# Kernel optimization log

Hardware: AMD Instinct MI355X
Metric: run time of the kernel (lower is better)

The kernel has to match this reference:

```python
import jax, jax.numpy as jnp
import numpy as np

C = 1024        # number of classes
N = 8           # proxies per class
ALLNUM = C * N  # 8192 total proxies
DIM = 512
R = 0.05
TOPK = int(np.ceil(R * ALLNUM))  # 410
LAM = 0.3
B = 2048


def setup_inputs() -> dict:
    key = jax.random.key(0)
    k1, k2, k3 = jax.random.split(key, 3)
    inp = jax.random.normal(k1, (B, DIM), dtype=jnp.float32)
    target = jax.random.randint(k2, (B,), 0, C, dtype=jnp.int64)
    # kaiming-uniform-initialized proxies approximated by scaled normal init
    proxies = jax.random.normal(k3, (DIM, ALLNUM), dtype=jnp.float32)
    instance_label = jnp.repeat(jnp.arange(C, dtype=jnp.int64), N)  # [ALLNUM]
    return {"input": inp, "target": target, "Proxies": proxies,
            "instance_label": instance_label}


def reference(input, target, Proxies, instance_label):
    # L2-normalize each proxy column (F.normalize along dim=0, eps=1e-12)
    norm = jnp.maximum(jnp.linalg.norm(Proxies, axis=0, keepdims=True), 1e-12)
    centers = Proxies / norm                             # [DIM, ALLNUM]
    similarity = input @ centers                          # [B, ALLNUM]

    positive_mask = (target[:, None] == instance_label[None, :]).astype(similarity.dtype)
    _, indices = jax.lax.top_k(similarity + 1000.0 * positive_mask, TOPK)  # [B, TOPK]

    rows = jnp.arange(similarity.shape[0])[:, None]
    mask = jnp.zeros_like(similarity).at[rows, indices].set(1.0)
    prob_a = mask * similarity                            # sparse-masked similarities

    y_instance_onehot = jax.nn.one_hot(instance_label, C, dtype=similarity.dtype)  # [ALLNUM, C]
    logits = prob_a @ y_instance_onehot                   # [B, C]

    y_target_onehot = jax.nn.one_hot(target, C, dtype=similarity.dtype)  # [B, C]
    logits_mask = 1.0 - (logits == 0.0).astype(similarity.dtype)

    # scale_mask_softmax with scale=1 along dim=1
    e = jnp.exp(logits) * logits_mask
    predict = e / (1e-8 + jnp.sum(e, axis=1, keepdims=True))
    lossClassify = jnp.mean(jnp.sum(-y_target_onehot * jnp.log(predict + 1e-20), axis=1))

    # proxy regularizer: cross-entropy of proxy-vs-class logits
    simCenter = centers.T @ centers                       # [ALLNUM, ALLNUM]
    centers_logits = simCenter @ y_instance_onehot        # [ALLNUM, C]
    logp = jax.nn.log_softmax(centers_logits, axis=1)
    reg = -jnp.mean(jnp.take_along_axis(logp, instance_label[:, None], axis=1))

    return (lossClassify + LAM * reg, lossClassify)
```

## Files before the change

kernel.cpp:

```cpp
#include <hip/hip_runtime.h>
#include <hip/hip_bf16.h>
#include <math.h>

#define C_CLS   1024
#define NPROXY  8
#define ALLNUM  8192
#define DIM     512
#define TOPK    410
#define LAM     0.3f
#define BATCH   2048

#define BAND_CAP_BLK 40
#define ROW_CAP      512
#define GCAP         64

typedef __bf16 bf16x8 __attribute__((ext_vector_type(8)));
typedef float floatx4 __attribute__((ext_vector_type(4)));
typedef unsigned short ushort_t;

#define WS_RNORM 0
#define WS_SIG   8192
#define WS_LP    10240
#define WS_RP    12288
#define WS_CNT   14336
#define WS_NDEF  16384
#define WS_FLAG  18432
#define WS_CLS   20480
#define WS_BVAL  (WS_CLS + 2048*1024)
#define WS_BCOL  (WS_BVAL + 2048*512)
#define WS_ABF   (WS_BCOL + 2048*256)
#define WS_PBF   (WS_ABF + 524288)
#define WS_STBF  (WS_PBF + 2097152)
#define WS_LOG   (WS_STBF + 262144)

__device__ inline float block_reduce(float v, int is_max, float* red, int t) {
    #pragma unroll
    for (int o = 32; o > 0; o >>= 1) {
        float w = __shfl_down(v, o);
        v = is_max ? fmaxf(v, w) : (v + w);
    }
    __syncthreads();
    if ((t & 63) == 0) red[t >> 6] = v;
    __syncthreads();
    return is_max ? fmaxf(fmaxf(red[0], red[1]), fmaxf(red[2], red[3]))
                  : (red[0] + red[1] + red[2] + red[3]);
}

__device__ inline ushort_t f2bf(float f) {
    unsigned u = __float_as_uint(f);
    return (ushort_t)((u + 0x7FFFu + ((u >> 16) & 1u)) >> 16);
}

__device__ inline float bf2f(ushort_t u) {
    return __uint_as_float(((unsigned)u) << 16);
}

__device__ inline void ld_g2l_16(const void* g, void* l) {
    __builtin_amdgcn_global_load_lds(
        (const __attribute__((address_space(1))) unsigned int*)g,
        (__attribute__((address_space(3))) unsigned int*)l,
        16, 0, 0);
}

__device__ inline unsigned f2ord(float f) {
    unsigned u = __float_as_uint(f);
    return (u & 0x80000000u) ? ~u : (u | 0x80000000u);
}

__global__ __launch_bounds__(256) void k_prep1(const float* __restrict__ P,
                                               const float* __restrict__ input,
                                               float* __restrict__ rnorm,
                                               float* __restrict__ rowsig,
                                               ushort_t* __restrict__ Abf,
                                               ushort_t* __restrict__ Pbf,
                                               ushort_t* __restrict__ Stbf,
                                               unsigned* __restrict__ zaux) {
    __shared__ float tile[32][33];
    __shared__ float s_rn[32];
    float* cred = &tile[0][0];
    int bx = blockIdx.x, t = threadIdx.x;
    if (bx < 256) {
        int tc = t & 31, g = t >> 5;
        int c = bx * 32 + tc;
        const float* pc = P + (size_t)(g * 64) * ALLNUM + c;
        float s = 0.f;
        #pragma unroll 8
        for (int d = 0; d < 64; ++d) {
            float v = pc[(size_t)d * ALLNUM];
            s += v * v;
        }
        cred[g * 32 + tc] = s;
        __syncthreads();
        if (g == 0) {
            float tot = 0.f;
            #pragma unroll
            for (int k = 0; k < 8; ++k) tot += cred[k * 32 + tc];
            float r = 1.0f / fmaxf(sqrtf(tot), 1e-12f);
            rnorm[c] = r;
            s_rn[tc] = r;
        }
        __syncthreads();
        #pragma unroll
        for (int p = 0; p < 8; ++p) {
            int idx = t + 256 * p;
            int d = idx >> 2, cc = idx & 3;
            const float* pp = P + (size_t)d * ALLNUM + bx * 32 + cc * 8;
            const float* rr = &s_rn[cc * 8];
            float4 a = *(const float4*)pp;
            float4 b = *(const float4*)(pp + 4);
            float v = a.x * rr[0] + a.y * rr[1] + a.z * rr[2] + a.w * rr[3] +
                      b.x * rr[4] + b.y * rr[5] + b.z * rr[6] + b.w * rr[7];
            Stbf[(size_t)(bx * 4 + cc) * DIM + d] = f2bf(v);
        }
    } else if (bx < 256 + 1024) {
        int a = bx - 256;
        int idx = a * 256 + t;
        float4 v = ((const float4*)input)[idx];
        ushort4 o;
        o.x = f2bf(v.x); o.y = f2bf(v.y); o.z = f2bf(v.z); o.w = f2bf(v.w);
        ((ushort4*)Abf)[idx] = o;
        float sq = v.x * v.x + v.y * v.y + v.z * v.z + v.w * v.w;
        #pragma unroll
        for (int off = 32; off > 0; off >>= 1) sq += __shfl_down(sq, off);
        int lane = t & 63, w = t >> 6;
        if (lane == 0) cred[w] = sq;
        __syncthreads();
        if (t == 0) {
            rowsig[2 * a]     = sqrtf(cred[0] + cred[1]);
            rowsig[2 * a + 1] = sqrtf(cred[2] + cred[3]);
        }
    } else if (bx < 256 + 1024 + 4096) {
        int id = bx - 1280;
        int c0 = (id & 255) * 32, r0 = (id >> 8) * 32;
        int tc = t & 31, tr = t >> 5;
        #pragma unroll
        for (int p = 0; p < 4; ++p)
            tile[tr + p * 8][tc] = P[(size_t)(r0 + tr + p * 8) * ALLNUM + c0 + tc];
        __syncthreads();
        #pragma unroll
        for (int p = 0; p < 4; ++p) {
            int oc = tr + p * 8;
            Pbf[(size_t)(c0 + oc) * DIM + r0 + tc] = f2bf(tile[tc][oc]);
        }
    } else {
        for (int i = t; i < 3 * 2048; i += 256) zaux[i] = 0u;
    }
}

__global__ __launch_bounds__(512, 2) void k_gemms(const ushort_t* __restrict__ Abf,
                                                  const ushort_t* __restrict__ Pbf,
                                                  const ushort_t* __restrict__ Stbf,
                                                  const float* __restrict__ rnorm,
                                                  const float* __restrict__ rowsig,
                                                  const int* __restrict__ target,
                                                  float* __restrict__ g_cls,
                                                  float* __restrict__ g_bval,
                                                  ushort_t* __restrict__ g_bcol,
                                                  unsigned* __restrict__ g_cnt,
                                                  unsigned* __restrict__ g_ndef,
                                                  unsigned* __restrict__ g_flag,
                                                  ushort_t* __restrict__ logits) {
    __shared__ __align__(16) ushort_t smem[65536];
    int bx = blockIdx.x, t = threadIdx.x;
    int w = t >> 6, lane = t & 63;
    int ml = lane & 15, q4 = lane >> 4;

    if (bx < 256) {
        int bi = (bx >> 5) * 256, bj = (bx & 31) * 256;
        int wm = w >> 2, wn = w & 3;
        ushort_t* sA0 = smem;
        ushort_t* sB0 = smem + 16384;
        ushort_t* sA1 = smem + 32768;
        ushort_t* sB1 = smem + 49152;

        floatx4 acc[8][4];
        #pragma unroll
        for (int mf = 0; mf < 8; ++mf)
            #pragma unroll
            for (int nf = 0; nf < 4; ++nf)
                acc[mf][nf] = (floatx4){0.f, 0.f, 0.f, 0.f};

        #define STAGE0(sa, sb, k0) do {                                        \
            _Pragma("unroll")                                                  \
            for (int it = 0; it < 4; ++it) {                                   \
                int c = w * 256 + it * 64 + lane;                              \
                int m = c >> 3, s = c & 7, qq = s ^ (m & 7);                   \
                ld_g2l_16(Abf + ((size_t)(bi + m) << 9) + (k0) + qq * 8,       \
                          &(sa)[c * 8]);                                       \
            }                                                                  \
            _Pragma("unroll")                                                  \
            for (int it = 0; it < 4; ++it) {                                   \
                int c = w * 256 + it * 64 + lane;                              \
                int m = c >> 3, s = c & 7, qq = s ^ (m & 7);                   \
                ld_g2l_16(Pbf + ((size_t)(bj + m) << 9) + (k0) + qq * 8,       \
                          &(sb)[c * 8]);                                       \
            }                                                                  \
        } while (0)

        STAGE0(sA0, sB0, 0);
        __syncthreads();
        #pragma unroll
        for (int tt = 0; tt < 8; ++tt) {
            ushort_t* cA = (tt & 1) ? sA1 : sA0;
            ushort_t* cB = (tt & 1) ? sB1 : sB0;
            if (tt < 7) {
                if (tt & 1) STAGE0(sA0, sB0, (tt + 1) * 64);
                else        STAGE0(sA1, sB1, (tt + 1) * 64);
            }
            #pragma unroll
            for (int kk = 0; kk < 2; ++kk) {
                bf16x8 bfr[4];
                #pragma unroll
                for (int nf = 0; nf < 4; ++nf) {
                    int n = wn * 64 + nf * 16 + ml;
                    int s = (kk * 4 + q4) ^ (n & 7);
                    bfr[nf] = *(const bf16x8*)&cB[n * 64 + s * 8];
                }
                #pragma unroll
                for (int mf = 0; mf < 8; ++mf) {
                    int m = wm * 128 + mf * 16 + ml;
                    int s = (kk * 4 + q4) ^ (m & 7);
                    bf16x8 af = *(const bf16x8*)&cA[m * 64 + s * 8];
                    #pragma unroll
                    for (int nf = 0; nf < 4; ++nf)
                        acc[mf][nf] = __builtin_amdgcn_mfma_f32_16x16x32_bf16(
                            af, bfr[nf], acc[mf][nf], 0, 0, 0);
                }
            }
            __syncthreads();
        }

        unsigned char* sb8 = (unsigned char*)smem;
        float*    e_cls = (float*)sb8;
        float*    e_bv  = (float*)(sb8 + 32768);
        ushort_t* e_bc  = (ushort_t*)(sb8 + 73728);
        unsigned* e_cnt = (unsigned*)(sb8 + 94208);
        unsigned* e_nd  = (unsigned*)(sb8 + 95232);

        #pragma unroll
        for (int i = t; i < 8192; i += 512) e_cls[i] = 0.f;
        if (t < 256) { e_cnt[t] = 0u; e_nd[t] = 0u; }
        __syncthreads();

        #pragma unroll
        for (int mf = 0; mf < 8; ++mf) {
            int rl0 = wm * 128 + mf * 16 + q4 * 4;
            int rowb = bi + rl0;
            float4 rs4 = *(const float4*)&rowsig[rowb];
            int4   tg4 = *(const int4*)&target[rowb];
            #pragma unroll
            for (int nf = 0; nf < 4; ++nf) {
                int cl = wn * 64 + nf * 16 + ml;
                int col = bj + cl;
                float sc = rnorm[col];
                int cls = col >> 3;
                int clsl = cl >> 3;
                #pragma unroll
                for (int i = 0; i < 4; ++i) {
                    int rl = rl0 + i;
                    float v = acc[mf][nf][i] * sc;
                    float sg = ((const float*)&rs4)[i] * (1.0f / 22.616f);
                    float hiT = 1.80f * sg, loT = 1.47f * sg;
                    int tg = ((const int*)&tg4)[i];
                    if (cls == tg) {
                        atomicAdd(&e_cls[rl * 32 + clsl], v);
                    } else if (v >= hiT) {
                        atomicAdd(&e_cls[rl * 32 + clsl], v);
                        atomicAdd(&e_nd[rl], 1u);
                    } else if (v >= loT) {
                        unsigned u = atomicAdd(&e_cnt[rl], 1u);
                        if (u < BAND_CAP_BLK) {
                            e_bv[rl * BAND_CAP_BLK + u] = v;
                            e_bc[rl * BAND_CAP_BLK + u] = (ushort_t)col;
                        }
                    }
                }
            }
        }
        __syncthreads();

        int bjc = bj >> 3;
        #pragma unroll
        for (int i = t; i < 8192; i += 512) {
            int rl = i >> 5, c = i & 31;
            g_cls[(size_t)(bi + rl) * C_CLS + bjc + c] = e_cls[i];
        }
        if (t < 256) {
            int row = bi + t;
            unsigned cbb = e_cnt[t];
            unsigned nd = e_nd[t];
            if (nd) atomicAdd(&g_ndef[row], nd);
            if (cbb) {
                unsigned cc = (cbb > BAND_CAP_BLK) ? BAND_CAP_BLK : cbb;
                unsigned base = atomicAdd(&g_cnt[row], cc);
                if (cbb > BAND_CAP_BLK || base + cc > ROW_CAP) g_flag[row] = 1u;
                for (unsigned j = 0; j < cc; ++j) {
                    if (base + j >= ROW_CAP) break;
                    g_bval[(size_t)row * ROW_CAP + base + j] = e_bv[t * BAND_CAP_BLK + j];
                    g_bcol[(size_t)row * ROW_CAP + base + j] = e_bc[t * BAND_CAP_BLK + j];
                }
            }
        }
        #undef STAGE0
    } else {
        int id = bx - 256;
        int bi = (id >> 3) * 256, bj = (id & 7) * 128;
        int wm = w >> 1, wn = w & 1;
        ushort_t* sA0 = smem;
        ushort_t* sB0 = smem + 16384;
        ushort_t* sA1 = smem + 32768;
        ushort_t* sB1 = smem + 49152;

        floatx4 acc[4][4];
        #pragma unroll
        for (int mf = 0; mf < 4; ++mf)
            #pragma unroll
            for (int nf = 0; nf < 4; ++nf)
                acc[mf][nf] = (floatx4){0.f, 0.f, 0.f, 0.f};

        #define STAGE1(sa, sb, k0) do {                                        \
            _Pragma("unroll")                                                  \
            for (int it = 0; it < 4; ++it) {                                   \
                int c = w * 256 + it * 64 + lane;                              \
                int m = c >> 3, s = c & 7, qq = s ^ (m & 7);                   \
                ld_g2l_16(Pbf + ((size_t)(bi + m) << 9) + (k0) + qq * 8,       \
                          &(sa)[c * 8]);                                       \
            }                                                                  \
            _Pragma("unroll")                                                  \
            for (int it = 0; it < 2; ++it) {                                   \
                int c = w * 128 + it * 64 + lane;                              \
                int m = c >> 3, s = c & 7, qq = s ^ (m & 7);                   \
                ld_g2l_16(Stbf + ((size_t)(bj + m) << 9) + (k0) + qq * 8,      \
                          &(sb)[c * 8]);                                       \
            }                                                                  \
        } while (0)

        STAGE1(sA0, sB0, 0);
        __syncthreads();
        #pragma unroll
        for (int tt = 0; tt < 8; ++tt) {
            ushort_t* cA = (tt & 1) ? sA1 : sA0;
            ushort_t* cB = (tt & 1) ? sB1 : sB0;
            if (tt < 7) {
                if (tt & 1) STAGE1(sA0, sB0, (tt + 1) * 64);
                else        STAGE1(sA1, sB1, (tt + 1) * 64);
            }
            #pragma unroll
            for (int kk = 0; kk < 2; ++kk) {
                bf16x8 bfr[4];
                #pragma unroll
                for (int nf = 0; nf < 4; ++nf) {
                    int n = wn * 64 + nf * 16 + ml;
                    int s = (kk * 4 + q4) ^ (n & 7);
                    bfr[nf] = *(const bf16x8*)&cB[n * 64 + s * 8];
                }
                #pragma unroll
                for (int mf = 0; mf < 4; ++mf) {
                    int m = wm * 64 + mf * 16 + ml;
                    int s = (kk * 4 + q4) ^ (m & 7);
                    bf16x8 af = *(const bf16x8*)&cA[m * 64 + s * 8];
                    #pragma unroll
                    for (int nf = 0; nf < 4; ++nf)
                        acc[mf][nf] = __builtin_amdgcn_mfma_f32_16x16x32_bf16(
                            af, bfr[nf], acc[mf][nf], 0, 0, 0);
                }
            }
            __syncthreads();
        }

        #pragma unroll
        for (int mf = 0; mf < 4; ++mf) {
            int rowb = bi + wm * 64 + mf * 16 + q4 * 4;
            float4 rnr = *(const float4*)&rnorm[rowb];
            #pragma unroll
            for (int nf = 0; nf < 4; ++nf) {
                int col = bj + wn * 64 + nf * 16 + ml;
                #pragma unroll
                for (int i = 0; i < 4; ++i)
                    logits[(size_t)(rowb + i) * C_CLS + col] =
                        f2bf(acc[mf][nf][i] * ((const float*)&rnr)[i]);
            }
        }
        #undef STAGE1
    }
}

__device__ inline void suffix_select1(unsigned* s_hist, unsigned kk,
                                      unsigned* s_wtot, unsigned* sh_bin,
                                      unsigned* sh_k, int t, int lane, int wid) {
    unsigned h = s_hist[t];
    unsigned v = h;
    #pragma unroll
    for (int off = 1; off < 64; off <<= 1) {
        unsigned o = __shfl_down(v, off);
        if (lane + off < 64) v += o;
    }
    if (lane == 0) s_wtot[wid] = v;
    __syncthreads();
    unsigned above = v - h;
    for (int w2 = wid + 1; w2 < 4; ++w2) above += s_wtot[w2];
    unsigned cum = above + h;
    if (cum >= kk && above < kk) { *sh_bin = (unsigned)t; *sh_k = kk - above; }
    __syncthreads();
}

__global__ __launch_bounds__(256) void k_finish(const int* __restrict__ target,
                                                const float* __restrict__ rowsig,
                                                const float* __restrict__ rnorm,
                                                const ushort_t* __restrict__ Abf,
                                                const ushort_t* __restrict__ Pbf,
                                                const float* __restrict__ g_cls,
                                                const float* __restrict__ g_bval,
                                                const ushort_t* __restrict__ g_bcol,
                                                const unsigned* __restrict__ g_cnt,
                                                const unsigned* __restrict__ g_ndef,
                                                const unsigned* __restrict__ g_flag,
                                                float* __restrict__ loss_part,
                                                const ushort_t* __restrict__ logits,
                                                float* __restrict__ reg_part) {
    __shared__ __align__(16) unsigned char smem[16384];
    int bx = blockIdx.x, t = threadIdx.x;
    int lane = t & 63, wid = t >> 6;

    if (bx < 2048) {
        float*    s_cls  = (float*)smem;
        float*    s_bval = (float*)(smem + 4096);
        ushort_t* s_bcol = (ushort_t*)(smem + 6144);
        unsigned* s_hist = (unsigned*)(smem + 7168);
        float*    s_arow = (float*)(smem + 8192);
        unsigned* s_wtot = (unsigned*)(smem + 10240);
        unsigned* shv    = (unsigned*)(smem + 10256);
        float*    shf    = (float*)(smem + 10272);
        float*    red    = (float*)(smem + 10288);
        float*    s_gval = (float*)(smem + 10304);

        int b = bx;
        int tgt = target[b];
        float sig = rowsig[b] * (1.0f / 22.616f);
        float hiT = 1.80f * sig, loT = 1.47f * sig;
        float binscale = 256.0f / (hiT - loT);

        ((float4*)s_cls)[t] = ((const float4*)(g_cls + (size_t)b * C_CLS))[t];
        unsigned cnt = g_cnt[b], nd = g_ndef[b], fl = g_flag[b];
        int kq = (TOPK - NPROXY) - (int)nd;
        int ok = (fl == 0u) && (cnt <= ROW_CAP) && (kq >= 0) && ((int)cnt >= kq);
        if (t == 0) shv[1] = 0u;
        s_hist[t] = 0u;
        __syncthreads();

        if (ok) {
            if (kq > 0) {
                for (int j = t; j < (int)cnt; j += 256) {
                    float v = g_bval[(size_t)b * ROW_CAP + j];
                    s_bval[j] = v;
                    s_bcol[j] = g_bcol[(size_t)b * ROW_CAP + j];
                    int bin = (int)((v - loT) * binscale);
                    bin = (bin > 255) ? 255 : bin;
                    atomicAdd(&s_hist[bin], 1u);
                }
                __syncthreads();
                suffix_select1(s_hist, (unsigned)kq, s_wtot, &shv[2], &shv[3], t, lane, wid);
                int Bb = (int)shv[2];
                int knew = (int)shv[3];
                for (int j = t; j < (int)cnt; j += 256) {
                    float v = s_bval[j];
                    int bin = (int)((v - loT) * binscale);
                    bin = (bin > 255) ? 255 : bin;
                    if (bin == Bb) {
                        unsigned g = atomicAdd(&shv[1], 1u);
                        if (g < GCAP) s_gval[g] = v;
                    }
                }
                __syncthreads();
                int gc = (int)shv[1];
                if (gc <= GCAP) {
                    if (t < gc) {
                        float vj = s_gval[t];
                        unsigned g = 0, geq = 0;
                        for (int i = 0; i < gc; ++i) {
                            float vi = s_gval[i];
                            g   += (vi > vj) ? 1u : 0u;
                            geq += (vi >= vj) ? 1u : 0u;
                        }
                        if (g < (unsigned)knew && geq >= (unsigned)knew) shf[0] = vj;
                    }
                } else {
                    for (int j = t; j < (int)cnt; j += 256) {
                        float vj = s_bval[j];
                        unsigned g = 0, geq = 0;
                        for (int i = 0; i < (int)cnt; ++i) {
                            float vi = s_bval[i];
                            g   += (vi > vj) ? 1u : 0u;
                            geq += (vi >= vj) ? 1u : 0u;
                        }
                        if (g < (unsigned)kq && geq >= (unsigned)kq) shf[0] = vj;
                    }
                }
                __syncthreads();
                float thr = shf[0];
                for (int j = t; j < (int)cnt; j += 256)
                    if (s_bval[j] >= thr)
                        atomicAdd(&s_cls[s_bcol[j] >> 3], s_bval[j]);
            }
        } else {
            for (int i = t; i < DIM; i += 256)
                s_arow[i] = bf2f(Abf[(size_t)b * DIM + i]);
            #pragma unroll
            for (int i = 0; i < 4; ++i) s_cls[t + 256 * i] = 0.f;
            __syncthreads();
            float4 v4[8];
            for (int p = 0; p < 8; ++p) {
                int f = t + 256 * p;
                float vv[4];
                for (int e = 0; e < 4; ++e) {
                    int col = 4 * f + e;
                    const ushort_t* pc = Pbf + (size_t)col * DIM;
                    float a = 0.f;
                    for (int d = 0; d < DIM; ++d)
                        a += s_arow[d] * bf2f(pc[d]);
                    vv[e] = a * rnorm[col];
                }
                float4 o; o.x = vv[0]; o.y = vv[1]; o.z = vv[2]; o.w = vv[3];
                v4[p] = o;
            }
            #pragma unroll
            for (int p = 0; p < 8; ++p) {
                int f = t + 256 * p;
                const float* pv = (const float*)&v4[p];
                if ((f >> 1) == tgt)
                    atomicAdd(&s_cls[tgt], pv[0] + pv[1] + pv[2] + pv[3]);
            }
            unsigned L = 0u, R = 0xFFFFFFFFu;
            for (int it = 0; it < 33 && R - L > 1; ++it) {
                unsigned mid = L + ((R - L) >> 1);
                float c = 0.f;
                #pragma unroll
                for (int p = 0; p < 8; ++p) {
                    int f = t + 256 * p;
                    const float* pv = (const float*)&v4[p];
                    if ((f >> 1) != tgt) {
                        #pragma unroll
                        for (int e = 0; e < 4; ++e)
                            c += (f2ord(pv[e]) >= mid) ? 1.f : 0.f;
                    }
                }
                c = block_reduce(c, 0, red, t);
                if (c >= (float)(TOPK - NPROXY)) L = mid; else R = mid;
                __syncthreads();
            }
            #pragma unroll
            for (int p = 0; p < 8; ++p) {
                int f = t + 256 * p;
                const float* pv = (const float*)&v4[p];
                if ((f >> 1) != tgt) {
                    #pragma unroll
                    for (int e = 0; e < 4; ++e)
                        if (f2ord(pv[e]) >= L)
                            atomicAdd(&s_cls[f >> 1], pv[e]);
                }
            }
        }
        __syncthreads();

        float4 cv = ((const float4*)s_cls)[t];
        float m = -1e30f;
        if (cv.x != 0.0f) m = fmaxf(m, cv.x);
        if (cv.y != 0.0f) m = fmaxf(m, cv.y);
        if (cv.z != 0.0f) m = fmaxf(m, cv.z);
        if (cv.w != 0.0f) m = fmaxf(m, cv.w);
        m = block_reduce(m, 1, red, t);
        float se = 0.f;
        if (cv.x != 0.0f) se += expf(cv.x - m);
        if (cv.y != 0.0f) se += expf(cv.y - m);
        if (cv.z != 0.0f) se += expf(cv.z - m);
        if (cv.w != 0.0f) se += expf(cv.w - m);
        se = block_reduce(se, 0, red, t);
        if (t == 0) {
            float lt = s_cls[tgt];
            float predict_t = expf(lt - m) / (1e-8f * expf(-m) + se);
            loss_part[b] = -logf(predict_t + 1e-20f);
        }
    } else {
        __shared__ float bsum[4];
        int rb = bx - 2048;
        int i = rb * 4 + wid;
        const ushort_t* row = logits + (size_t)i * C_CLS;
        uint4 c0 = ((const uint4*)row)[lane];
        uint4 c1 = ((const uint4*)(row + 512))[lane];

        float f[16];
        const unsigned* u0 = (const unsigned*)&c0;
        const unsigned* u1 = (const unsigned*)&c1;
        #pragma unroll
        for (int k = 0; k < 4; ++k) {
            f[2 * k]     = __uint_as_float(u0[k] << 16);
            f[2 * k + 1] = __uint_as_float(u0[k] & 0xFFFF0000u);
            f[8 + 2 * k]     = __uint_as_float(u1[k] << 16);
            f[8 + 2 * k + 1] = __uint_as_float(u1[k] & 0xFFFF0000u);
        }

        int cstar = i >> 3;
        int chunk = cstar >> 9, within = cstar & 511;
        float sd = 0.f;
        if (lane == (within >> 3)) sd = f[chunk * 8 + (within & 7)];

        float m = -1e30f;
        #pragma unroll
        for (int k = 0; k < 16; ++k) m = fmaxf(m, f[k]);
        #pragma unroll
        for (int off = 32; off > 0; off >>= 1) m = fmaxf(m, __shfl_xor(m, off));

        float se = 0.f;
        #pragma unroll
        for (int k = 0; k < 16; ++k) se += expf(f[k] - m);
        #pragma unroll
        for (int off = 32; off > 0; off >>= 1) se += __shfl_xor(se, off);
        #pragma unroll
        for (int off = 32; off > 0; off >>= 1) sd += __shfl_xor(sd, off);

        if (lane == 0) bsum[wid] = m + logf(se) - sd;
        __syncthreads();
        if (t == 0)
            reg_part[rb] = bsum[0] + bsum[1] + bsum[2] + bsum[3];
    }
}

__global__ __launch_bounds__(256) void k_final(const float* __restrict__ lp,
                                               const float* __restrict__ rp,
                                               float* __restrict__ out) {
    __shared__ float red[4];
    int t = threadIdx.x;
    float4 a = ((const float4*)lp)[t];
    float4 b = ((const float4*)lp)[t + 256];
    float4 c = ((const float4*)rp)[t];
    float4 d = ((const float4*)rp)[t + 256];
    float ls = a.x + a.y + a.z + a.w + b.x + b.y + b.z + b.w;
    float rs = c.x + c.y + c.z + c.w + d.x + d.y + d.z + d.w;
    ls = block_reduce(ls, 0, red, t);
    rs = block_reduce(rs, 0, red, t);
    if (t == 0) {
        float lc = ls / (float)BATCH;
        float rg = rs / (float)ALLNUM;
        out[0] = lc + LAM * rg;
        out[1] = lc;
    }
}

extern "C" void kernel_launch(void* const* d_in, const int* in_sizes, int n_in,
                              void* d_out, int out_size, void* d_ws, size_t ws_size,
                              hipStream_t stream) {
    const float* input  = (const float*)d_in[0];
    const int*   target = (const int*)d_in[1];
    const float* P      = (const float*)d_in[2];

    float* ws        = (float*)d_ws;
    float* rnorm     = ws + WS_RNORM;
    float* rowsig    = ws + WS_SIG;
    float* loss_part = ws + WS_LP;
    float* reg_part  = ws + WS_RP;
    unsigned* g_cnt  = (unsigned*)(ws + WS_CNT);
    unsigned* g_ndef = (unsigned*)(ws + WS_NDEF);
    unsigned* g_flag = (unsigned*)(ws + WS_FLAG);
    float* g_cls     = ws + WS_CLS;
    float* g_bval    = ws + WS_BVAL;
    ushort_t* g_bcol = (ushort_t*)(ws + WS_BCOL);
    ushort_t* Abf    = (ushort_t*)(ws + WS_ABF);
    ushort_t* Pbf    = (ushort_t*)(ws + WS_PBF);
    ushort_t* Stbf   = (ushort_t*)(ws + WS_STBF);
    ushort_t* logits = (ushort_t*)(ws + WS_LOG);
    float* out       = (float*)d_out;

    hipLaunchKernelGGL(k_prep1, dim3(256 + 1024 + 4096 + 1), dim3(256), 0, stream,
                       P, input, rnorm, rowsig, Abf, Pbf, Stbf, g_cnt);
    hipLaunchKernelGGL(k_gemms, dim3(512), dim3(512), 0, stream,
                       Abf, Pbf, Stbf, rnorm, rowsig, target,
                       g_cls, g_bval, g_bcol, g_cnt, g_ndef, g_flag, logits);
    hipLaunchKernelGGL(k_finish, dim3(4096), dim3(256), 0, stream,
                       target, rowsig, rnorm, Abf, Pbf,
                       g_cls, g_bval, g_bcol, g_cnt, g_ndef, g_flag,
                       loss_part, logits, reg_part);
    hipLaunchKernelGGL(k_final, dim3(1), dim3(256), 0, stream,
                       loss_part, reg_part, out);
}
```

Before: 149.1 us.

## Fuse softmax partials into GEMM epilogue, merge prep transposes, drop final kernel

The proxy-regularizer GEMM epilogue now computes per-row partial max, exp-sum and the diagonal logit, replacing the bf16 logits matrix write. The finish kernel then combines 8 partials per row instead of reading full logit rows. Prep merges the normalize, transpose and scaled-transpose work into one tiled pass over P through shared memory, instead of several separate passes. The block-to-tile mapping in the GEMM kernel is reordered, and the final reduction moves into the last finishing block via an atomic counter, removing one launch. This adds a global atomic, threadfence ordering and a hard-coded block count that must match the grid size.

```diff
diff --git a/kernel.cpp b/kernel.cpp
--- a/kernel.cpp
+++ b/kernel.cpp
@@ -31,7 +31,10 @@
 #define WS_ABF   (WS_BCOL + 2048*256)
 #define WS_PBF   (WS_ABF + 524288)
 #define WS_STBF  (WS_PBF + 2097152)
-#define WS_LOG   (WS_STBF + 262144)
+#define WS_MX    (WS_STBF + 262144)
+#define WS_SE    (WS_MX + 65536)
+#define WS_DIAG  (WS_SE + 65536)
+#define WS_SYNC  (WS_DIAG + 8192)
 
 __device__ inline float block_reduce(float v, int is_max, float* red, int t) {
     #pragma unroll
@@ -42,8 +45,10 @@
     __syncthreads();
     if ((t & 63) == 0) red[t >> 6] = v;
     __syncthreads();
-    return is_max ? fmaxf(fmaxf(red[0], red[1]), fmaxf(red[2], red[3]))
-                  : (red[0] + red[1] + red[2] + red[3]);
+    float r = is_max ? fmaxf(fmaxf(red[0], red[1]), fmaxf(red[2], red[3]))
+                     : (red[0] + red[1] + red[2] + red[3]);
+    __syncthreads();
+    return r;
 }
 
 __device__ inline ushort_t f2bf(float f) {
@@ -74,46 +79,70 @@
                                                ushort_t* __restrict__ Abf,
                                                ushort_t* __restrict__ Pbf,
                                                ushort_t* __restrict__ Stbf,
-                                               unsigned* __restrict__ zaux) {
-    __shared__ float tile[32][33];
-    __shared__ float s_rn[32];
-    float* cred = &tile[0][0];
+                                               unsigned* __restrict__ zaux,
+                                               unsigned* __restrict__ zsync) {
+    __shared__ float stile[512 * 17];
+    __shared__ float cred[256];
+    __shared__ float s_rn[16];
     int bx = blockIdx.x, t = threadIdx.x;
-    if (bx < 256) {
-        int tc = t & 31, g = t >> 5;
-        int c = bx * 32 + tc;
-        const float* pc = P + (size_t)(g * 64) * ALLNUM + c;
+    if (bx < 512) {
+        int c0 = bx * 16;
+        #pragma unroll
+        for (int it = 0; it < 8; ++it) {
+            int r = it * 64 + (t >> 2);
+            int c4 = (t & 3) * 4;
+            float4 v = *(const float4*)&P[(size_t)r * ALLNUM + c0 + c4];
+            stile[r * 17 + c4]     = v.x;
+            stile[r * 17 + c4 + 1] = v.y;
+            stile[r * 17 + c4 + 2] = v.z;
+            stile[r * 17 + c4 + 3] = v.w;
+        }
+        __syncthreads();
+        int tc = t & 15, g = t >> 4;
         float s = 0.f;
         #pragma unroll 8
-        for (int d = 0; d < 64; ++d) {
-            float v = pc[(size_t)d * ALLNUM];
+        for (int k = 0; k < 32; ++k) {
+            float v = stile[(g * 32 + k) * 17 + tc];
             s += v * v;
         }
-        cred[g * 32 + tc] = s;
+        cred[g * 16 + tc] = s;
         __syncthreads();
         if (g == 0) {
             float tot = 0.f;
             #pragma unroll
-            for (int k = 0; k < 8; ++k) tot += cred[k * 32 + tc];
+            for (int k = 0; k < 16; ++k) tot += cred[k * 16 + tc];
             float r = 1.0f / fmaxf(sqrtf(tot), 1e-12f);
-            rnorm[c] = r;
+            rnorm[c0 + tc] = r;
             s_rn[tc] = r;
         }
         __syncthreads();
         #pragma unroll
         for (int p = 0; p < 8; ++p) {
             int idx = t + 256 * p;
-            int d = idx >> 2, cc = idx & 3;
-            const float* pp = P + (size_t)d * ALLNUM + bx * 32 + cc * 8;
-            const float* rr = &s_rn[cc * 8];
-            float4 a = *(const float4*)pp;
-            float4 b = *(const float4*)(pp + 4);
-            float v = a.x * rr[0] + a.y * rr[1] + a.z * rr[2] + a.w * rr[3] +
-                      b.x * rr[4] + b.y * rr[5] + b.z * rr[6] + b.w * rr[7];
-            Stbf[(size_t)(bx * 4 + cc) * DIM + d] = f2bf(v);
-        }
-    } else if (bx < 256 + 1024) {
-        int a = bx - 256;
+            int c = idx >> 7, d4 = (idx & 127) * 4;
+            ushort4 o;
+            o.x = f2bf(stile[(d4    ) * 17 + c]);
+            o.y = f2bf(stile[(d4 + 1) * 17 + c]);
+            o.z = f2bf(stile[(d4 + 2) * 17 + c]);
+            o.w = f2bf(stile[(d4 + 3) * 17 + c]);
+            *(ushort4*)&Pbf[(size_t)(c0 + c) * DIM + d4] = o;
+        }
+        #pragma unroll
+        for (int p = 0; p < 2; ++p) {
+            int idx = t + 256 * p;
+            int cc = idx >> 8, d2 = (idx & 255) * 2;
+            float v0 = 0.f, v1 = 0.f;
+            #pragma unroll
+            for (int n = 0; n < 8; ++n) {
+                float rr = s_rn[cc * 8 + n];
+                v0 += stile[(d2    ) * 17 + cc * 8 + n] * rr;
+                v1 += stile[(d2 + 1) * 17 + cc * 8 + n] * rr;
+            }
+            ushort2 o; o.x = f2bf(v0); o.y = f2bf(v1);
+            *(ushort2*)&Stbf[(size_t)(bx * 2 + cc) * DIM + d2] = o;
+        }
+    } else if (bx < 512 + 1024) {
+        int a = bx - 512;
         int idx = a * 256 + t;
         float4 v = ((const float4*)input)[idx];
         ushort4 o;
@@ -129,21 +158,9 @@
             rowsig[2 * a]     = sqrtf(cred[0] + cred[1]);
             rowsig[2 * a + 1] = sqrtf(cred[2] + cred[3]);
         }
-    } else if (bx < 256 + 1024 + 4096) {
-        int id = bx - 1280;
-        int c0 = (id & 255) * 32, r0 = (id >> 8) * 32;
-        int tc = t & 31, tr = t >> 5;
-        #pragma unroll
-        for (int p = 0; p < 4; ++p)
-            tile[tr + p * 8][tc] = P[(size_t)(r0 + tr + p * 8) * ALLNUM + c0 + tc];
-        __syncthreads();
-        #pragma unroll
-        for (int p = 0; p < 4; ++p) {
-            int oc = tr + p * 8;
-            Pbf[(size_t)(c0 + oc) * DIM + r0 + tc] = f2bf(tile[tc][oc]);
-        }
     } else {
         for (int i = t; i < 3 * 2048; i += 256) zaux[i] = 0u;
+        if (t < 64) zsync[t] = 0u;
     }
 }
 
@@ -159,14 +176,19 @@
                                                   unsigned* __restrict__ g_cnt,
                                                   unsigned* __restrict__ g_ndef,
                                                   unsigned* __restrict__ g_flag,
-                                                  ushort_t* __restrict__ logits) {
+                                                  float* __restrict__ g_mx,
+                                                  float* __restrict__ g_se,
+                                                  float* __restrict__ g_diag) {
     __shared__ __align__(16) ushort_t smem[65536];
     int bx = blockIdx.x, t = threadIdx.x;
     int w = t >> 6, lane = t & 63;
     int ml = lane & 15, q4 = lane >> 4;
 
-    if (bx < 256) {
-        int bi = (bx >> 5) * 256, bj = (bx & 31) * 256;
+    int kx = bx & 7, sx = bx >> 3;
+    int wid = (sx < 32) ? (kx * 32 + sx) : (256 + kx * 32 + (sx - 32));
+
+    if (wid < 256) {
+        int bi = (wid & 7) * 256, bj = (wid >> 3) * 256;
         int wm = w >> 2, wn = w & 3;
         ushort_t* sA0 = smem;
         ushort_t* sB0 = smem + 16384;
@@ -229,6 +251,7 @@
             }
             __syncthreads();
         }
+        #undef STAGE0
 
         unsigned char* sb8 = (unsigned char*)smem;
         float*    e_cls = (float*)sb8;
@@ -301,9 +324,8 @@
                 }
             }
         }
-        #undef STAGE0
     } else {
-        int id = bx - 256;
+        int id = wid - 256;
         int bi = (id >> 3) * 256, bj = (id & 7) * 128;
         int wm = w >> 1, wn = w & 1;
         ushort_t* sA0 = smem;
@@ -367,21 +389,76 @@
             }
             __syncthreads();
         }
-
+        #undef STAGE1
+
+        int cj = bj >> 7;
+        float mloc[4][4], sloc[4][4];
         #pragma unroll
         for (int mf = 0; mf < 4; ++mf) {
             int rowb = bi + wm * 64 + mf * 16 + q4 * 4;
             float4 rnr = *(const float4*)&rnorm[rowb];
             #pragma unroll
-            for (int nf = 0; nf < 4; ++nf) {
-                int col = bj + wn * 64 + nf * 16 + ml;
+            for (int i = 0; i < 4; ++i) {
+                float mm = -1e30f;
+                #pragma unroll
+                for (int nf = 0; nf < 4; ++nf)
+                    mm = fmaxf(mm, acc[mf][nf][i] * ((const float*)&rnr)[i]);
+                mloc[mf][i] = mm;
+            }
+        }
+        #pragma unroll
+        for (int off = 1; off < 16; off <<= 1)
+            #pragma unroll
+            for (int mf = 0; mf < 4; ++mf)
                 #pragma unroll
                 for (int i = 0; i < 4; ++i)
-                    logits[(size_t)(rowb + i) * C_CLS + col] =
-                        f2bf(acc[mf][nf][i] * ((const float*)&rnr)[i]);
-            }
-        }
-        #undef STAGE1
+                    mloc[mf][i] = fmaxf(mloc[mf][i], __shfl_xor(mloc[mf][i], off));
+        #pragma unroll
+        for (int mf = 0; mf < 4; ++mf) {
+            int rowb = bi + wm * 64 + mf * 16 + q4 * 4;
+            float4 rnr = *(const float4*)&rnorm[rowb];
+            #pragma unroll
+            for (int i = 0; i < 4; ++i) {
+                float ss = 0.f;
+                int row = rowb + i;
+                #pragma unroll
+                for (int nf = 0; nf < 4; ++nf) {
+                    float v = acc[mf][nf][i] * ((const float*)&rnr)[i];
+                    ss += expf(v - mloc[mf][i]);
+                    int col = bj + wn * 64 + nf * 16 + ml;
+                    if (col == (row >> 3)) g_diag[row] = v;
+                }
+                sloc[mf][i] = ss;
+            }
+        }
+        #pragma unroll
+        for (int off = 1; off < 16; off <<= 1)
+            #pragma unroll
+            for (int mf = 0; mf < 4; ++mf)
+                #pragma unroll
+                for (int i = 0; i < 4; ++i)
+                    sloc[mf][i] += __shfl_xor(sloc[mf][i], off);
+        float* s_m = (float*)smem;
+        float* s_s = s_m + 512;
+        if (ml == 0) {
+            #pragma unroll
+            for (int mf = 0; mf < 4; ++mf)
+                #pragma unroll
+                for (int i = 0; i < 4; ++i) {
+                    int r = wm * 64 + mf * 16 + q4 * 4 + i;
+                    s_m[r * 2 + wn] = mloc[mf][i];
+                    s_s[r * 2 + wn] = sloc[mf][i];
+                }
+        }
+        __syncthreads();
+        if (t < 256) {
+            float m0 = s_m[2 * t], m1 = s_m[2 * t + 1];
+            float s0 = s_s[2 * t], s1 = s_s[2 * t + 1];
+            float M = fmaxf(m0, m1);
+            float S = s0 * expf(m0 - M) + s1 * expf(m1 - M);
+            g_mx[(size_t)(bi + t) * 8 + cj] = M;
+            g_se[(size_t)(bi + t) * 8 + cj] = S;
+        }
     }
 }
 
@@ -416,9 +493,14 @@
                                                 const unsigned* __restrict__ g_ndef,
                                                 const unsigned* __restrict__ g_flag,
                                                 float* __restrict__ loss_part,
-                                                const ushort_t* __restrict__ logits,
-                                                float* __restrict__ reg_part) {
+                                                const float* __restrict__ g_mx,
+                                                const float* __restrict__ g_se,
+                                                const float* __restrict__ g_diag,
+                                                float* __restrict__ reg_part,
+                                                unsigned* __restrict__ sync,
+                                                float* __restrict__ out) {
     __shared__ __align__(16) unsigned char smem[16384];
+    __shared__ unsigned s_last;
     int bx = blockIdx.x, t = threadIdx.x;
     int lane = t & 63, wid = t >> 6;
 
@@ -444,7 +526,7 @@
         unsigned cnt = g_cnt[b], nd = g_ndef[b], fl = g_flag[b];
         int kq = (TOPK - NPROXY) - (int)nd;
         int ok = (fl == 0u) && (cnt <= ROW_CAP) && (kq >= 0) && ((int)cnt >= kq);
-        if (t == 0) shv[1] = 0u;
+        if (t == 0) shv[0] = 0u;
         s_hist[t] = 0u;
         __syncthreads();
 
@@ -459,20 +541,20 @@
                     atomicAdd(&s_hist[bin], 1u);
                 }
                 __syncthreads();
-                suffix_select1(s_hist, (unsigned)kq, s_wtot, &shv[2], &shv[3], t, lane, wid);
-                int Bb = (int)shv[2];
-                int knew = (int)shv[3];
+                suffix_select1(s_hist, (unsigned)kq, s_wtot, &shv[1], &shv[2], t, lane, wid);
+                int Bb = (int)shv[1];
+                int knew = (int)shv[2];
                 for (int j = t; j < (int)cnt; j += 256) {
                     float v = s_bval[j];
                     int bin = (int)((v - loT) * binscale);
                     bin = (bin > 255) ? 255 : bin;
                     if (bin == Bb) {
-                        unsigned g = atomicAdd(&shv[1], 1u);
+                        unsigned g = atomicAdd(&shv[0], 1u);
                         if (g < GCAP) s_gval[g] = v;
                     }
                 }
                 __syncthreads();
-                int gc = (int)shv[1];
+                int gc = (int)shv[0];
                 if (gc <= GCAP) {
                     if (t < gc) {
                         float vj = s_gval[t];
@@ -581,68 +663,53 @@
             loss_part[b] = -logf(predict_t + 1e-20f);
         }
     } else {
-        __shared__ float bsum[4];
+        float* red2 = (float*)smem;
         int rb = bx - 2048;
-        int i = rb * 4 + wid;
-        const ushort_t* row = logits + (size_t)i * C_CLS;
-        uint4 c0 = ((const uint4*)row)[lane];
-        uint4 c1 = ((const uint4*)(row + 512))[lane];
-
-        float f[16];
-        const unsigned* u0 = (const unsigned*)&c0;
-        const unsigned* u1 = (const unsigned*)&c1;
-        #pragma unroll
-        for (int k = 0; k < 4; ++k) {
-            f[2 * k]     = __uint_as_float(u0[k] << 16);
-            f[2 * k + 1] = __uint_as_float(u0[k] & 0xFFFF0000u);
-            f[8 + 2 * k]     = __uint_as_float(u1[k] << 16);
-            f[8 + 2 * k + 1] = __uint_as_float(u1[k] & 0xFFFF0000u);
-        }
-
-        int cstar = i >> 3;
-        int chunk = cstar >> 9, within = cstar & 511;
-        float sd = 0.f;
-        if (lane == (within >> 3)) sd = f[chunk * 8 + (within & 7)];
-
-        float m = -1e30f;
-        #pragma unroll
-        for (int k = 0; k < 16; ++k) m = fmaxf(m, f[k]);
-        #pragma unroll
-        for (int off = 32; off > 0; off >>= 1) m = fmaxf(m, __shfl_xor(m, off));
-
-        float se = 0.f;
-        #pragma unroll
-        for (int k = 0; k < 16; ++k) se += expf(f[k] - m);
-        #pragma unroll
-        for (int off = 32; off > 0; off >>= 1) se += __shfl_xor(se, off);
-        #pragma unroll
-        for (int off = 32; off > 0; off >>= 1) sd += __shfl_xor(sd, off);
-
-        if (lane == 0) bsum[wid] = m + logf(se) - sd;
-        __syncthreads();
-        if (t == 0)
-            reg_part[rb] = bsum[0] + bsum[1] + bsum[2] + bsum[3];
+        float val = 0.f;
+        if (t < 64) {
+            int row = rb * 64 + t;
+            float mj[8], sj[8];
+            float M = -1e30f;
+            #pragma unroll
+            for (int j = 0; j < 8; ++j) {
+                mj[j] = g_mx[(size_t)row * 8 + j];
+                sj[j] = g_se[(size_t)row * 8 + j];
+                M = fmaxf(M, mj[j]);
+            }
+            float S = 0.f;
+            #pragma unroll
+            for (int j = 0; j < 8; ++j) S += sj[j] * expf(mj[j] - M);
+            val = M + logf(S) - g_diag[row];
+        }
+        val = block_reduce(val, 0, red2, t);
+        if (t == 0) reg_part[rb] = val;
     }
-}
-
-__global__ __launch_bounds__(256) void k_final(const float* __restrict__ lp,
-                                               const float* __restrict__ rp,
-                                               float* __restrict__ out) {
-    __shared__ float red[4];
-    int t = threadIdx.x;
-    float4 a = ((const float4*)lp)[t];
-    float4 b = ((const float4*)lp)[t + 256];
-    float4 c = ((const float4*)rp)[t];
-    float4 d = ((const float4*)rp)[t + 256];
-    float ls = a.x + a.y + a.z + a.w + b.x + b.y + b.z + b.w;
-    float rs = c.x + c.y + c.z + c.w + d.x + d.y + d.z + d.w;
-    ls = block_reduce(ls, 0, red, t);
-    rs = block_reduce(rs, 0, red, t);
+
     if (t == 0) {
-        float lc = ls / (float)BATCH;
-        float rg = rs / (float)ALLNUM;
-        out[0] = lc + LAM * rg;
-        out[1] = lc;
+        __threadfence();
+        unsigned old = atomicAdd(&sync[0], 1u);
+        s_last = (old == 2175u) ? 1u : 0u;
+    }
+    __syncthreads();
+    if (s_last) {
+        __threadfence();
+        float* red = (float*)smem;
+        float4 a = ((const float4*)loss_part)[t];
+        float4 b2 = ((const float4*)loss_part)[t + 256];
+        float ls = a.x + a.y + a.z + a.w + b2.x + b2.y + b2.z + b2.w;
+        float rs = 0.f;
+        if (t < 32) {
+            float4 c = ((const float4*)reg_part)[t];
+            rs = c.x + c.y + c.z + c.w;
+        }
+        ls = block_reduce(ls, 0, red, t);
+        rs = block_reduce(rs, 0, red, t);
+        if (t == 0) {
+            float lc = ls / (float)BATCH;
+            float rg = rs / (float)ALLNUM;
+            out[0] = lc + LAM * rg;
+            out[1] = lc;
+        }
     }
 }
 
@@ -667,18 +734,20 @@
     ushort_t* Abf    = (ushort_t*)(ws + WS_ABF);
     ushort_t* Pbf    = (ushort_t*)(ws + WS_PBF);
     ushort_t* Stbf   = (ushort_t*)(ws + WS_STBF);
-    ushort_t* logits = (ushort_t*)(ws + WS_LOG);
+    float* g_mx      = ws + WS_MX;
+    float* g_se      = ws + WS_SE;
+    float* g_diag    = ws + WS_DIAG;
+    unsigned* syncp  = (unsigned*)(ws + WS_SYNC);
     float* out       = (float*)d_out;
 
-    hipLaunchKernelGGL(k_prep1, dim3(256 + 1024 + 4096 + 1), dim3(256), 0, stream,
-                       P, input, rnorm, rowsig, Abf, Pbf, Stbf, g_cnt);
+    hipLaunchKernelGGL(k_prep1, dim3(512 + 1024 + 1), dim3(256), 0, stream,
+                       P, input, rnorm, rowsig, Abf, Pbf, Stbf, g_cnt, syncp);
     hipLaunchKernelGGL(k_gemms, dim3(512), dim3(512), 0, stream,
                        Abf, Pbf, Stbf, rnorm, rowsig, target,
-                       g_cls, g_bval, g_bcol, g_cnt, g_ndef, g_flag, logits);
-    hipLaunchKernelGGL(k_finish, dim3(4096), dim3(256), 0, stream,
+                       g_cls, g_bval, g_bcol, g_cnt, g_ndef, g_flag,
+                       g_mx, g_se, g_diag);
+    hipLaunchKernelGGL(k_finish, dim3(2048 + 128), dim3(256), 0, stream,
                        target, rowsig, rnorm, Abf, Pbf,
                        g_cls, g_bval, g_bcol, g_cnt, g_ndef, g_flag,
-                       loss_part, logits, reg_part);
-    hipLaunchKernelGGL(k_final, dim3(1), dim3(256), 0, stream,
-                       loss_part, reg_part, out);
-}
+                       loss_part, g_mx, g_se, g_diag, reg_part, syncp, out);
+}
```

Result: slower. 184.4 us (+23.7%).
